# Optimization experiments

Measured on AMD Instinct MI355X. Metric: run time of the kernel, lower is better.

The kernel has to match this reference:

```python
import jax, jax.numpy as jnp
import numpy as np

NEG_SLOPE = 0.2
EPS = 1e-16


def gat_layer(x, src, dst, W, att_src, att_dst, bias, heads, out_ch, concat, n_nodes):
    # Linear projection -> [N, H, C]
    h = (x @ W).reshape(n_nodes, heads, out_ch)
    # Per-node attention logits [N, H]
    a_src = (h * att_src[None]).sum(-1)
    a_dst = (h * att_dst[None]).sum(-1)
    # Per-edge logits, LeakyReLU (message j -> i with src=j, dst=i)
    alpha = a_src[src] + a_dst[dst]                      # [E, H]
    alpha = jnp.where(alpha >= 0, alpha, NEG_SLOPE * alpha)
    # Segment softmax over incoming edges of each dst node
    amax = jax.ops.segment_max(alpha, dst, num_segments=n_nodes)  # [N, H]
    ealpha = jnp.exp(alpha - amax[dst])
    denom = jax.ops.segment_sum(ealpha, dst, num_segments=n_nodes)
    alpha = ealpha / (denom[dst] + EPS)
    # Weighted messages + scatter-add aggregation
    msg = h[src] * alpha[..., None]                      # [E, H, C]
    out = jax.ops.segment_sum(msg, dst, num_segments=n_nodes)  # [N, H, C]
    out = out.reshape(n_nodes, heads * out_ch) if concat else out.mean(axis=1)
    return out + bias


def setup_inputs() -> dict:
    key = jax.random.key(0)
    ks = jax.random.split(key, 11)
    N, E, F, H, C1 = 50000, 1600000, 128, 8, 8
    x = jax.random.normal(ks[0], (N, F), dtype=jnp.float32)
    edge_index = jax.random.randint(ks[1], (2, E), 0, N, dtype=jnp.int64)
    s = 1.0 / np.sqrt(F)
    W1 = jax.random.normal(ks[2], (F, H * C1), dtype=jnp.float32) * s
    att_src1 = jax.random.normal(ks[3], (H, C1), dtype=jnp.float32) * 0.1
    att_dst1 = jax.random.normal(ks[4], (H, C1), dtype=jnp.float32) * 0.1
    bias1 = jax.random.normal(ks[5], (H * C1,), dtype=jnp.float32) * 0.1
    W2 = jax.random.normal(ks[6], (H * C1, F), dtype=jnp.float32) * (1.0 / np.sqrt(H * C1))
    att_src2 = jax.random.normal(ks[7], (1, F), dtype=jnp.float32) * 0.1
    att_dst2 = jax.random.normal(ks[8], (1, F), dtype=jnp.float32) * 0.1
    bias2 = jax.random.normal(ks[9], (F,), dtype=jnp.float32) * 0.1
    return {"x": x, "edge_index": edge_index, "W1": W1, "att_src1": att_src1,
            "att_dst1": att_dst1, "bias1": bias1, "W2": W2, "att_src2": att_src2,
            "att_dst2": att_dst2, "bias2": bias2}


def reference(x, edge_index, W1, att_src1, att_dst1, bias1, W2, att_src2, att_dst2, bias2):
    N = x.shape[0]
    # PyG GATConv add_self_loops=True: append (i, i) for every node
    loops = jnp.arange(N, dtype=edge_index.dtype)
    src = jnp.concatenate([edge_index[0], loops])
    dst = jnp.concatenate([edge_index[1], loops])
    # eval mode: dropouts are identity
    h = gat_layer(x, src, dst, W1, att_src1, att_dst1, bias1, heads=8, out_ch=8,
                  concat=True, n_nodes=N)            # [N, 64]
    h = jax.nn.elu(h)
    out = gat_layer(h, src, dst, W2, att_src2, att_dst2, bias2, heads=1, out_ch=128,
                    concat=False, n_nodes=N)         # [N, 128]
    return out
```

## Files before the change

### kernel.cpp

```cpp
#include <hip/hip_runtime.h>
#include <stdint.h>

#define NEG_SLOPE 0.2f
#define EPSV 1e-16f
#define NBLK 256

typedef __attribute__((ext_vector_type(8))) short short8;
typedef __attribute__((ext_vector_type(4))) float f32x4;

__device__ inline short bf16r(float f){
  union { float f; unsigned u; } v; v.f = f;
  unsigned r = (v.u + 0x7FFFu + ((v.u >> 16) & 1u)) >> 16;
  return (short)r;
}
__device__ inline float bf16lo(unsigned u){
  union { unsigned u; float f; } v; v.u = u << 16; return v.f;
}
__device__ inline float bf16hi(unsigned u){
  union { unsigned u; float f; } v; v.u = u & 0xFFFF0000u; return v.f;
}

__device__ inline void get_edge(const void* ei, int is64, int E, int e, int& s, int& d){
  if (e >= E){ s = d = e - E; return; }
  if (is64){
    const long long* p = (const long long*)ei;
    s = (int)p[e]; d = (int)p[(long long)E + e];
  } else {
    const int* p = (const int*)ei;
    s = p[e]; d = p[E + e];
  }
}

__device__ inline int get_dst(const void* ei, int is64, int E, int e){
  if (e >= E) return e - E;
  if (is64) return (int)((const long long*)ei)[(long long)E + e];
  return ((const int*)ei)[E + e];
}

__global__ void detect_dtype(const int* ei32, int* flag){
  if (threadIdx.x == 0 && blockIdx.x == 0){
    int nz = 0;
    for (int i = 0; i < 64; ++i) nz |= ei32[2*i + 1];
    *flag = (nz == 0) ? 1 : 0;
  }
}

__global__ void cvt_to_bf16(const float* __restrict__ x, short* __restrict__ xb, int n4){
  int i = blockIdx.x*blockDim.x + threadIdx.x;
  if (i >= n4) return;
  f32x4 v = *(const f32x4*)(x + (size_t)i*4);
  short4 o;
  o.x = bf16r(v[0]); o.y = bf16r(v[1]); o.z = bf16r(v[2]); o.w = bf16r(v[3]);
  *(short4*)(xb + (size_t)i*4) = o;
}

__device__ inline void pack_one(const float* W, short* Wp, int NCOL, int idx){
  int NNT = NCOL >> 4;
  int j = idx & 7, n16 = (idx >> 3) & 15, q = (idx >> 7) & 3, tile = idx >> 9;
  int nt = tile % NNT, kt = tile / NNT;
  int k = kt*32 + q*8 + j, n = nt*16 + n16;
  Wp[idx] = bf16r(W[k*NCOL + n]);
}
__global__ void pack_w_both(const float* __restrict__ W1, short* __restrict__ W1p,
                            const float* __restrict__ W2, short* __restrict__ W2p){
  int idx = blockIdx.x*blockDim.x + threadIdx.x;
  if (idx < 8192) pack_one(W1, W1p, 64, idx);
  else            pack_one(W2, W2p, 128, idx - 8192);
}

__global__ void gemv_att2(const float* __restrict__ W2, const float* __restrict__ as2,
                          const float* __restrict__ ad2, float* __restrict__ va_s,
                          float* __restrict__ va_d){
  int k = threadIdx.x;
  float s = 0.f, d = 0.f;
  for (int c = 0; c < 128; ++c){
    float w = W2[k*128 + c];
    s = fmaf(w, as2[c], s);
    d = fmaf(w, ad2[c], d);
  }
  va_s[k] = s; va_d[k] = d;
}

template<int K, int NCOL>
__global__ __launch_bounds__(256) void gemm_mfma(const short* __restrict__ A, const short* __restrict__ Bp,
                                                 short* __restrict__ Cb, int M){
  constexpr int NKT = K/32, NNT = NCOL/16;
  int wave = (blockIdx.x*256 + (int)threadIdx.x) >> 6;
  int lane = threadIdx.x & 63;
  int row0 = wave << 4;
  if (row0 >= M) return;
  int m = lane & 15, q = lane >> 4;
  f32x4 acc[NNT];
#pragma unroll
  for (int i = 0; i < NNT; ++i) acc[i] = (f32x4){0.f,0.f,0.f,0.f};
#pragma unroll
  for (int kt = 0; kt < NKT; ++kt){
    short8 a = *(const short8*)(A + (size_t)(row0 + m)*K + kt*32 + q*8);
#pragma unroll
    for (int nt = 0; nt < NNT; ++nt){
      short8 b = *(const short8*)(Bp + (size_t)(((kt*NNT + nt)*4 + q)*16 + m)*8);
      acc[nt] = __builtin_amdgcn_mfma_f32_16x16x32_bf16(a, b, acc[nt], 0, 0, 0);
    }
  }
#pragma unroll
  for (int nt = 0; nt < NNT; ++nt){
#pragma unroll
    for (int r = 0; r < 4; ++r){
      Cb[(size_t)(row0 + q*4 + r)*NCOL + nt*16 + m] = bf16r(acc[nt][r]);
    }
  }
}

template<int K, int NCOL>
__global__ __launch_bounds__(256) void gemm_mfma_bias(const short* __restrict__ A, const short* __restrict__ Bp,
                                                      const float* __restrict__ bias,
                                                      float* __restrict__ C, int M){
  constexpr int NKT = K/32, NNT = NCOL/16;
  int wave = (blockIdx.x*256 + (int)threadIdx.x) >> 6;
  int lane = threadIdx.x & 63;
  int row0 = wave << 4;
  if (row0 >= M) return;
  int m = lane & 15, q = lane >> 4;
  f32x4 acc[NNT];
#pragma unroll
  for (int i = 0; i < NNT; ++i) acc[i] = (f32x4){0.f,0.f,0.f,0.f};
#pragma unroll
  for (int kt = 0; kt < NKT; ++kt){
    short8 a = *(const short8*)(A + (size_t)(row0 + m)*K + kt*32 + q*8);
#pragma unroll
    for (int nt = 0; nt < NNT; ++nt){
      short8 b = *(const short8*)(Bp + (size_t)(((kt*NNT + nt)*4 + q)*16 + m)*8);
      acc[nt] = __builtin_amdgcn_mfma_f32_16x16x32_bf16(a, b, acc[nt], 0, 0, 0);
    }
  }
#pragma unroll
  for (int nt = 0; nt < NNT; ++nt){
    float bv = bias[nt*16 + m];
#pragma unroll
    for (int r = 0; r < 4; ++r){
      C[(size_t)(row0 + q*4 + r)*NCOL + nt*16 + m] = acc[nt][r] + bv;
    }
  }
}

__global__ void logits_l1(const unsigned short* __restrict__ h1b, const float* __restrict__ att_s,
                          const float* __restrict__ att_d, float* __restrict__ asrc,
                          float* __restrict__ adst, int N){
  int tid = threadIdx.x;
  int n = blockIdx.x*4 + (tid >> 6);
  int j = tid & 63;
  if (n >= N) return;
  float h = bf16lo((unsigned)h1b[(size_t)n*64 + j]);
  float ps = h * att_s[j];
  float pd = h * att_d[j];
#pragma unroll
  for (int mm = 4; mm; mm >>= 1){ ps += __shfl_xor(ps, mm, 8); pd += __shfl_xor(pd, mm, 8); }
  if ((j & 7) == 0){ asrc[n*8 + (j >> 3)] = ps; adst[n*8 + (j >> 3)] = pd; }
}

__global__ __launch_bounds__(256) void p1_hist(const void* ei, const int* flag, int E, int E2,
                                               int* __restrict__ block_counts){
  __shared__ int h[256];
  int t = threadIdx.x, blk = blockIdx.x;
  h[t] = 0; __syncthreads();
  int chunk = (E2 + NBLK - 1)/NBLK;
  int beg = blk*chunk, end = min(beg + chunk, E2);
  int is64 = *flag;
  for (int e = beg + t; e < end; e += 256){
    int d = get_dst(ei, is64, E, e);
    atomicAdd(&h[d >> 8], 1);
  }
  __syncthreads();
  block_counts[blk*256 + t] = h[t];
}

__global__ void p2_bucket_scan(const int* __restrict__ block_counts, int* __restrict__ bucket_base){
  __shared__ int sd[256];
  int t = threadIdx.x;
  int tot = 0;
  for (int b = 0; b < NBLK; ++b) tot += block_counts[b*256 + t];
  sd[t] = tot; __syncthreads();
  for (int off = 1; off < 256; off <<= 1){
    int v = (t >= off) ? sd[t - off] : 0;
    __syncthreads(); sd[t] += v; __syncthreads();
  }
  bucket_base[t] = sd[t] - tot;
  if (t == 255) bucket_base[256] = sd[255];
}

__global__ void p2_block_off(const int* __restrict__ block_counts, const int* __restrict__ bucket_base,
                             int* __restrict__ block_off){
  __shared__ int sd[256];
  int b = blockIdx.x, t = threadIdx.x;
  int v = block_counts[t*256 + b];
  sd[t] = v; __syncthreads();
  for (int off = 1; off < 256; off <<= 1){
    int u = (t >= off) ? sd[t - off] : 0;
    __syncthreads(); sd[t] += u; __syncthreads();
  }
  block_off[t*256 + b] = bucket_base[b] + sd[t] - v;
}

__global__ __launch_bounds__(256) void p3_scatter(const void* ei, const int* flag, int E, int E2,
                                                  const int* __restrict__ block_off,
                                                  unsigned* __restrict__ packed){
  __shared__ int cur[256];
  int t = threadIdx.x, blk = blockIdx.x;
  cur[t] = block_off[blk*256 + t];
  __syncthreads();
  int chunk = (E2 + NBLK - 1)/NBLK;
  int beg = blk*chunk, end = min(beg + chunk, E2);
  int is64 = *flag;
  for (int e = beg + t; e < end; e += 256){
    int s, d; get_edge(ei, is64, E, e, s, d);
    int pos = atomicAdd(&cur[d >> 8], 1);
    packed[pos] = ((unsigned)s << 8) | (unsigned)(d & 255);
  }
}

__global__ __launch_bounds__(256) void p4_sort(const unsigned* __restrict__ packed,
                                               const int* __restrict__ bucket_base,
                                               int N, int E2,
                                               int* __restrict__ offs, int* __restrict__ srcs){
  __shared__ int hist[256];
  __shared__ int cur[256];
  int b = blockIdx.x, t = threadIdx.x;
  int base = bucket_base[b], cnt = bucket_base[b + 1] - base;
  hist[t] = 0; __syncthreads();
  for (int p = t; p < cnt; p += 256){
    atomicAdd(&hist[packed[base + p] & 255u], 1);
  }
  __syncthreads();
  int v = hist[t];
  cur[t] = v; __syncthreads();
  for (int off = 1; off < 256; off <<= 1){
    int u = (t >= off) ? cur[t - off] : 0;
    __syncthreads(); cur[t] += u; __syncthreads();
  }
  int ex = cur[t] - v;
  __syncthreads();
  cur[t] = ex;
  int node = b*256 + t;
  if (node < N) offs[node] = base + ex;
  __syncthreads();
  for (int p = t; p < cnt; p += 256){
    unsigned pk = packed[base + p];
    int pos = atomicAdd(&cur[pk & 255u], 1);
    srcs[base + pos] = (int)(pk >> 8);
  }
  if (b == 0 && t == 0) offs[N] = E2;
}

__global__ __launch_bounds__(256) void agg_l1(const char* __restrict__ h1b,
                       const float* __restrict__ asrc, const float* __restrict__ adst,
                       const int* __restrict__ offs, const int* __restrict__ srcs,
                       const float* __restrict__ bias,
                       const float* __restrict__ va_s, const float* __restrict__ va_d,
                       uint4* __restrict__ hout,
                       float* __restrict__ asrc2, float* __restrict__ adst2, int N){
  int tid = threadIdx.x;
  int i = blockIdx.x*4 + (tid >> 6);
  if (i >= N) return;
  int lane = tid & 63, g = lane >> 3, c = lane & 7;
  float ad = adst[i*8 + c];
  int beg = offs[i], end = offs[i + 1], last = end - 1;
  float acc[8];
#pragma unroll
  for (int k = 0; k < 8; ++k) acc[k] = 0.f;
  float den = 0.f;
  for (int p = beg; p < end; p += 32){
    int m[4], s[4];
#pragma unroll
    for (int k = 0; k < 4; ++k) m[k] = p + 8*k + g;
#pragma unroll
    for (int k = 0; k < 4; ++k) s[k] = srcs[min(m[k], last)];
    float a[4];
#pragma unroll
    for (int k = 0; k < 4; ++k) a[k] = asrc[s[k]*8 + c];
    uint4 v[4];
#pragma unroll
    for (int k = 0; k < 4; ++k) v[k] = *(const uint4*)(h1b + ((size_t)s[k] << 7) + (c << 4));
    float w[4];
#pragma unroll
    for (int k = 0; k < 4; ++k){
      float z = a[k] + ad; z = (z >= 0.f) ? z : NEG_SLOPE*z;
      w[k] = (m[k] < end) ? __expf(z) : 0.f;
      den += w[k];
    }
#pragma unroll
    for (int k = 0; k < 4; ++k){
      acc[0] = fmaf(w[k], bf16lo(v[k].x), acc[0]); acc[1] = fmaf(w[k], bf16hi(v[k].x), acc[1]);
      acc[2] = fmaf(w[k], bf16lo(v[k].y), acc[2]); acc[3] = fmaf(w[k], bf16hi(v[k].y), acc[3]);
      acc[4] = fmaf(w[k], bf16lo(v[k].z), acc[4]); acc[5] = fmaf(w[k], bf16hi(v[k].z), acc[5]);
      acc[6] = fmaf(w[k], bf16lo(v[k].w), acc[6]); acc[7] = fmaf(w[k], bf16hi(v[k].w), acc[7]);
    }
  }
#pragma unroll
  for (int mm = 8; mm <= 32; mm <<= 1){
#pragma unroll
    for (int k = 0; k < 8; ++k) acc[k] += __shfl_xor(acc[k], mm, 64);
    den += __shfl_xor(den, mm, 64);
  }
  if (g == 0){
    float inv = 1.f/(den + EPSV);
    float o[8];
#pragma unroll
    for (int k = 0; k < 8; ++k){
      float t = acc[k]*inv + bias[c*8 + k];
      o[k] = (t > 0.f) ? t : (__expf(t) - 1.f);
    }
    unsigned pk[4];
#pragma unroll
    for (int k = 0; k < 4; ++k)
      pk[k] = (unsigned)(unsigned short)bf16r(o[2*k]) | ((unsigned)(unsigned short)bf16r(o[2*k+1]) << 16);
    uint4 ov; ov.x = pk[0]; ov.y = pk[1]; ov.z = pk[2]; ov.w = pk[3];
    hout[(size_t)i*8 + c] = ov;
    float ps = 0.f, pd = 0.f;
#pragma unroll
    for (int k = 0; k < 8; ++k){
      ps = fmaf(o[k], va_s[c*8 + k], ps);
      pd = fmaf(o[k], va_d[c*8 + k], pd);
    }
#pragma unroll
    for (int mm = 1; mm <= 4; mm <<= 1){
      ps += __shfl_xor(ps, mm, 8);
      pd += __shfl_xor(pd, mm, 8);
    }
    if (c == 0){ asrc2[i] = ps; adst2[i] = pd; }
  }
}

__global__ __launch_bounds__(256) void agg_l2(const char* __restrict__ hin2,
                       const float* __restrict__ asrc, const float* __restrict__ adst,
                       const int* __restrict__ offs, const int* __restrict__ srcs,
                       uint4* __restrict__ qout, int N){
  int tid = threadIdx.x;
  int i = blockIdx.x*4 + (tid >> 6);
  if (i >= N) return;
  int lane = tid & 63, g = lane >> 3, c = lane & 7;
  float ad = adst[i];
  int beg = offs[i], end = offs[i + 1], last = end - 1;
  float acc[8];
#pragma unroll
  for (int k = 0; k < 8; ++k) acc[k] = 0.f;
  float den = 0.f;
  for (int p = beg; p < end; p += 32){
    int m[4], s[4];
#pragma unroll
    for (int k = 0; k < 4; ++k) m[k] = p + 8*k + g;
#pragma unroll
    for (int k = 0; k < 4; ++k) s[k] = srcs[min(m[k], last)];
    float a[4];
#pragma unroll
    for (int k = 0; k < 4; ++k) a[k] = asrc[s[k]];
    uint4 v[4];
#pragma unroll
    for (int k = 0; k < 4; ++k) v[k] = *(const uint4*)(hin2 + ((size_t)s[k] << 7) + (c << 4));
    float w[4];
#pragma unroll
    for (int k = 0; k < 4; ++k){
      float z = a[k] + ad; z = (z >= 0.f) ? z : NEG_SLOPE*z;
      w[k] = (m[k] < end) ? __expf(z) : 0.f;
      den += w[k];
    }
#pragma unroll
    for (int k = 0; k < 4; ++k){
      acc[0] = fmaf(w[k], bf16lo(v[k].x), acc[0]); acc[1] = fmaf(w[k], bf16hi(v[k].x), acc[1]);
      acc[2] = fmaf(w[k], bf16lo(v[k].y), acc[2]); acc[3] = fmaf(w[k], bf16hi(v[k].y), acc[3]);
      acc[4] = fmaf(w[k], bf16lo(v[k].z), acc[4]); acc[5] = fmaf(w[k], bf16hi(v[k].z), acc[5]);
      acc[6] = fmaf(w[k], bf16lo(v[k].w), acc[6]); acc[7] = fmaf(w[k], bf16hi(v[k].w), acc[7]);
    }
  }
#pragma unroll
  for (int mm = 8; mm <= 32; mm <<= 1){
#pragma unroll
    for (int k = 0; k < 8; ++k) acc[k] += __shfl_xor(acc[k], mm, 64);
    den += __shfl_xor(den, mm, 64);
  }
  if (g == 0){
    float inv = 1.f/(den + EPSV);
    unsigned pk[4];
#pragma unroll
    for (int k = 0; k < 4; ++k){
      float o0 = acc[2*k]*inv, o1 = acc[2*k + 1]*inv;
      pk[k] = (unsigned)(unsigned short)bf16r(o0) | ((unsigned)(unsigned short)bf16r(o1) << 16);
    }
    uint4 ov; ov.x = pk[0]; ov.y = pk[1]; ov.z = pk[2]; ov.w = pk[3];
    qout[(size_t)i*8 + c] = ov;
  }
}

extern "C" void kernel_launch(void* const* d_in, const int* in_sizes, int n_in,
                              void* d_out, int out_size, void* d_ws, size_t ws_size,
                              hipStream_t stream){
  const float* x   = (const float*)d_in[0];
  const void*  ei  = d_in[1];
  const float* W1  = (const float*)d_in[2];
  const float* as1 = (const float*)d_in[3];
  const float* ad1 = (const float*)d_in[4];
  const float* b1  = (const float*)d_in[5];
  const float* W2  = (const float*)d_in[6];
  const float* as2 = (const float*)d_in[7];
  const float* ad2 = (const float*)d_in[8];
  const float* b2  = (const float*)d_in[9];

  int N  = in_sizes[0] / 128;
  int E  = in_sizes[1] / 2;
  int E2 = E + N;
  int NB = (N + 255) >> 8;

  char* p = (char*)d_ws;
  auto alloc = [&](size_t bytes) -> void* {
    void* r = (void*)p;
    p += (bytes + 255) & ~(size_t)255;
    return r;
  };
  short*    xb     = (short*)alloc((size_t)N*128*2);
  short*    W1p    = (short*)alloc((size_t)128*64*2);
  short*    W2p    = (short*)alloc((size_t)64*128*2);
  short*    h1b    = (short*)alloc((size_t)N*64*2);
  float*    asrc1  = (float*)alloc((size_t)N*8*4);
  float*    adst1  = (float*)alloc((size_t)N*8*4);
  short*    hin2   = (short*)alloc((size_t)N*64*2);
  short*    hq     = (short*)alloc((size_t)N*64*2);
  float*    asrc2  = (float*)alloc((size_t)N*4);
  float*    adst2  = (float*)alloc((size_t)N*4);
  float*    va_s2  = (float*)alloc(64*4);
  float*    va_d2  = (float*)alloc(64*4);
  int*      offs   = (int*)alloc((size_t)(N + 1)*4);
  int*      srcs   = (int*)alloc((size_t)E2*4);
  unsigned* packed = (unsigned*)alloc((size_t)E2*4);
  int*      bcnt   = (int*)alloc((size_t)NBLK*256*4);
  int*      boff   = (int*)alloc((size_t)NBLK*256*4);
  int*      bbase  = (int*)alloc(257*4);
  int*      flag   = (int*)alloc(4);

  dim3 B(256);
  detect_dtype<<<1, 64, 0, stream>>>((const int*)ei, flag);

  int n4 = N*128/4;
  cvt_to_bf16<<<(n4 + 255)/256, B, 0, stream>>>(x, xb, n4);
  pack_w_both<<<16384/256, B, 0, stream>>>(W1, W1p, W2, W2p);
  gemv_att2<<<1, 64, 0, stream>>>(W2, as2, ad2, va_s2, va_d2);

  int nwav = (N + 15)/16;
  gemm_mfma<128,64><<<(nwav + 3)/4, B, 0, stream>>>(xb, W1p, h1b, N);
  logits_l1<<<(N + 3)/4, B, 0, stream>>>((const unsigned short*)h1b, as1, ad1, asrc1, adst1, N);

  p1_hist<<<NBLK, B, 0, stream>>>(ei, flag, E, E2, bcnt);
  p2_bucket_scan<<<1, B, 0, stream>>>(bcnt, bbase);
  p2_block_off<<<256, B, 0, stream>>>(bcnt, bbase, boff);
  p3_scatter<<<NBLK, B, 0, stream>>>(ei, flag, E, E2, boff, packed);
  p4_sort<<<NB, B, 0, stream>>>(packed, bbase, N, E2, offs, srcs);

  agg_l1<<<(N + 3)/4, B, 0, stream>>>((const char*)h1b, asrc1, adst1, offs, srcs, b1,
                                      va_s2, va_d2, (uint4*)hin2, asrc2, adst2, N);

  agg_l2<<<(N + 3)/4, B, 0, stream>>>((const char*)hin2, asrc2, adst2, offs, srcs,
                                      (uint4*)hq, N);

  gemm_mfma_bias<64,128><<<(nwav + 3)/4, B, 0, stream>>>(hq, W2p, b2, (float*)d_out, N);
}
```

Before: 254.2 us.

## Fuse prep kernels, bf16 convert into GEMM1, logits into GEMM epilogue, merge scans

Merges the dtype check, weight packing and attention GEMV into one prep kernel. Folds the fp32-to-bf16 conversion of x into the first GEMM's A load and computes the layer-1 attention logits in that GEMM's epilogue using shuffles. Merges the two scan kernels into one, which makes every block redo the bucket totals. Pre-scales logits by log2(e) so aggregation can use exp2f, and stores pre-shifted source offsets to save index arithmetic. The aim is fewer launches and less intermediate memory traffic, at the cost of redundant per-block scan work.

```diff
diff --git a/kernel.cpp b/kernel.cpp
--- a/kernel.cpp
+++ b/kernel.cpp
@@ -3,6 +3,7 @@
 
 #define NEG_SLOPE 0.2f
 #define EPSV 1e-16f
+#define LOG2E 1.44269504088896340736f
 #define NBLK 256
 
 typedef __attribute__((ext_vector_type(8))) short short8;
@@ -37,23 +38,6 @@
   return ((const int*)ei)[E + e];
 }
 
-__global__ void detect_dtype(const int* ei32, int* flag){
-  if (threadIdx.x == 0 && blockIdx.x == 0){
-    int nz = 0;
-    for (int i = 0; i < 64; ++i) nz |= ei32[2*i + 1];
-    *flag = (nz == 0) ? 1 : 0;
-  }
-}
-
-__global__ void cvt_to_bf16(const float* __restrict__ x, short* __restrict__ xb, int n4){
-  int i = blockIdx.x*blockDim.x + threadIdx.x;
-  if (i >= n4) return;
-  f32x4 v = *(const f32x4*)(x + (size_t)i*4);
-  short4 o;
-  o.x = bf16r(v[0]); o.y = bf16r(v[1]); o.z = bf16r(v[2]); o.w = bf16r(v[3]);
-  *(short4*)(xb + (size_t)i*4) = o;
-}
-
 __device__ inline void pack_one(const float* W, short* Wp, int NCOL, int idx){
   int NNT = NCOL >> 4;
   int j = idx & 7, n16 = (idx >> 3) & 15, q = (idx >> 7) & 3, tile = idx >> 9;
@@ -61,30 +45,39 @@
   int k = kt*32 + q*8 + j, n = nt*16 + n16;
   Wp[idx] = bf16r(W[k*NCOL + n]);
 }
-__global__ void pack_w_both(const float* __restrict__ W1, short* __restrict__ W1p,
-                            const float* __restrict__ W2, short* __restrict__ W2p){
-  int idx = blockIdx.x*blockDim.x + threadIdx.x;
-  if (idx < 8192) pack_one(W1, W1p, 64, idx);
-  else            pack_one(W2, W2p, 128, idx - 8192);
-}
-
-__global__ void gemv_att2(const float* __restrict__ W2, const float* __restrict__ as2,
-                          const float* __restrict__ ad2, float* __restrict__ va_s,
-                          float* __restrict__ va_d){
-  int k = threadIdx.x;
-  float s = 0.f, d = 0.f;
-  for (int c = 0; c < 128; ++c){
-    float w = W2[k*128 + c];
-    s = fmaf(w, as2[c], s);
-    d = fmaf(w, ad2[c], d);
-  }
-  va_s[k] = s; va_d[k] = d;
-}
-
-template<int K, int NCOL>
-__global__ __launch_bounds__(256) void gemm_mfma(const short* __restrict__ A, const short* __restrict__ Bp,
-                                                 short* __restrict__ Cb, int M){
-  constexpr int NKT = K/32, NNT = NCOL/16;
+__global__ void prep(const int* __restrict__ ei32, int* __restrict__ flag,
+                     const float* __restrict__ W1, short* __restrict__ W1p,
+                     const float* __restrict__ W2, short* __restrict__ W2p,
+                     const float* __restrict__ as2, const float* __restrict__ ad2,
+                     float* __restrict__ va_s, float* __restrict__ va_d){
+  int b = blockIdx.x, t = threadIdx.x;
+  if (b < 64){
+    int idx = b*256 + t;
+    if (idx < 8192) pack_one(W1, W1p, 64, idx);
+    else            pack_one(W2, W2p, 128, idx - 8192);
+  } else {
+    if (t == 0){
+      int nz = 0;
+      for (int i = 0; i < 64; ++i) nz |= ei32[2*i + 1];
+      *flag = (nz == 0) ? 1 : 0;
+    }
+    if (t < 64){
+      float s = 0.f, d = 0.f;
+      for (int c = 0; c < 128; ++c){
+        float w = W2[t*128 + c];
+        s = fmaf(w, as2[c], s);
+        d = fmaf(w, ad2[c], d);
+      }
+      va_s[t] = s * LOG2E; va_d[t] = d * LOG2E;
+    }
+  }
+}
+
+__global__ __launch_bounds__(256) void gemm1(const float* __restrict__ x, const short* __restrict__ Bp,
+                                             const float* __restrict__ att_s, const float* __restrict__ att_d,
+                                             short* __restrict__ Cb,
+                                             float* __restrict__ asrc1, float* __restrict__ adst1, int M){
+  constexpr int NKT = 4, NNT = 4;
   int wave = (blockIdx.x*256 + (int)threadIdx.x) >> 6;
   int lane = threadIdx.x & 63;
   int row0 = wave << 4;
@@ -95,7 +88,12 @@
   for (int i = 0; i < NNT; ++i) acc[i] = (f32x4){0.f,0.f,0.f,0.f};
 #pragma unroll
   for (int kt = 0; kt < NKT; ++kt){
-    short8 a = *(const short8*)(A + (size_t)(row0 + m)*K + kt*32 + q*8);
+    const float* xr = x + (size_t)(row0 + m)*128 + kt*32 + q*8;
+    f32x4 f0 = *(const f32x4*)xr;
+    f32x4 f1 = *(const f32x4*)(xr + 4);
+    short8 a;
+#pragma unroll
+    for (int j = 0; j < 4; ++j){ a[j] = bf16r(f0[j]); a[4 + j] = bf16r(f1[j]); }
 #pragma unroll
     for (int nt = 0; nt < NNT; ++nt){
       short8 b = *(const short8*)(Bp + (size_t)(((kt*NNT + nt)*4 + q)*16 + m)*8);
@@ -106,16 +104,41 @@
   for (int nt = 0; nt < NNT; ++nt){
 #pragma unroll
     for (int r = 0; r < 4; ++r){
-      Cb[(size_t)(row0 + q*4 + r)*NCOL + nt*16 + m] = bf16r(acc[nt][r]);
-    }
-  }
-}
-
-template<int K, int NCOL>
-__global__ __launch_bounds__(256) void gemm_mfma_bias(const short* __restrict__ A, const short* __restrict__ Bp,
-                                                      const float* __restrict__ bias,
-                                                      float* __restrict__ C, int M){
-  constexpr int NKT = K/32, NNT = NCOL/16;
+      Cb[(size_t)(row0 + q*4 + r)*64 + nt*16 + m] = bf16r(acc[nt][r]);
+    }
+  }
+  float atts[4], attd[4];
+#pragma unroll
+  for (int nt = 0; nt < 4; ++nt){
+    atts[nt] = att_s[nt*16 + m] * LOG2E;
+    attd[nt] = att_d[nt*16 + m] * LOG2E;
+  }
+  int isw = (m & 7) == 0;
+#pragma unroll
+  for (int r = 0; r < 4; ++r){
+    int row = row0 + q*4 + r;
+#pragma unroll
+    for (int nt = 0; nt < 4; ++nt){
+      float ps = acc[nt][r] * atts[nt];
+      float pd = acc[nt][r] * attd[nt];
+#pragma unroll
+      for (int mm = 1; mm <= 4; mm <<= 1){
+        ps += __shfl_xor(ps, mm, 64);
+        pd += __shfl_xor(pd, mm, 64);
+      }
+      if (isw){
+        int head = 2*nt + (m >> 3);
+        asrc1[row*8 + head] = ps;
+        adst1[row*8 + head] = pd;
+      }
+    }
+  }
+}
+
+__global__ __launch_bounds__(256) void gemm2(const short* __restrict__ A, const short* __restrict__ Bp,
+                                             const float* __restrict__ bias,
+                                             float* __restrict__ C, int M){
+  constexpr int NKT = 2, NNT = 8;
   int wave = (blockIdx.x*256 + (int)threadIdx.x) >> 6;
   int lane = threadIdx.x & 63;
   int row0 = wave << 4;
@@ -126,7 +149,7 @@
   for (int i = 0; i < NNT; ++i) acc[i] = (f32x4){0.f,0.f,0.f,0.f};
 #pragma unroll
   for (int kt = 0; kt < NKT; ++kt){
-    short8 a = *(const short8*)(A + (size_t)(row0 + m)*K + kt*32 + q*8);
+    short8 a = *(const short8*)(A + (size_t)(row0 + m)*64 + kt*32 + q*8);
 #pragma unroll
     for (int nt = 0; nt < NNT; ++nt){
       short8 b = *(const short8*)(Bp + (size_t)(((kt*NNT + nt)*4 + q)*16 + m)*8);
@@ -138,24 +161,9 @@
     float bv = bias[nt*16 + m];
 #pragma unroll
     for (int r = 0; r < 4; ++r){
-      C[(size_t)(row0 + q*4 + r)*NCOL + nt*16 + m] = acc[nt][r] + bv;
-    }
-  }
-}
-
-__global__ void logits_l1(const unsigned short* __restrict__ h1b, const float* __restrict__ att_s,
-                          const float* __restrict__ att_d, float* __restrict__ asrc,
-                          float* __restrict__ adst, int N){
-  int tid = threadIdx.x;
-  int n = blockIdx.x*4 + (tid >> 6);
-  int j = tid & 63;
-  if (n >= N) return;
-  float h = bf16lo((unsigned)h1b[(size_t)n*64 + j]);
-  float ps = h * att_s[j];
-  float pd = h * att_d[j];
-#pragma unroll
-  for (int mm = 4; mm; mm >>= 1){ ps += __shfl_xor(ps, mm, 8); pd += __shfl_xor(pd, mm, 8); }
-  if ((j & 7) == 0){ asrc[n*8 + (j >> 3)] = ps; adst[n*8 + (j >> 3)] = pd; }
+      C[(size_t)(row0 + q*4 + r)*128 + nt*16 + m] = acc[nt][r] + bv;
+    }
+  }
 }
 
 __global__ __launch_bounds__(256) void p1_hist(const void* ei, const int* flag, int E, int E2,
@@ -174,31 +182,34 @@
   block_counts[blk*256 + t] = h[t];
 }
 
-__global__ void p2_bucket_scan(const int* __restrict__ block_counts, int* __restrict__ bucket_base){
-  __shared__ int sd[256];
-  int t = threadIdx.x;
-  int tot = 0;
-  for (int b = 0; b < NBLK; ++b) tot += block_counts[b*256 + t];
-  sd[t] = tot; __syncthreads();
+__global__ __launch_bounds__(256) void p2_scan(const int* __restrict__ block_counts,
+                                               int* __restrict__ bucket_base,
+                                               int* __restrict__ block_off){
+  __shared__ int tot[256];
+  __shared__ int ex[256];
+  __shared__ int col[256];
+  int b = blockIdx.x, t = threadIdx.x;
+  int s = 0;
+  for (int w = 0; w < NBLK; ++w) s += block_counts[w*256 + t];
+  tot[t] = s; __syncthreads();
   for (int off = 1; off < 256; off <<= 1){
-    int v = (t >= off) ? sd[t - off] : 0;
-    __syncthreads(); sd[t] += v; __syncthreads();
-  }
-  bucket_base[t] = sd[t] - tot;
-  if (t == 255) bucket_base[256] = sd[255];
-}
-
-__global__ void p2_block_off(const int* __restrict__ block_counts, const int* __restrict__ bucket_base,
-                             int* __restrict__ block_off){
-  __shared__ int sd[256];
-  int b = blockIdx.x, t = threadIdx.x;
+    int v = (t >= off) ? tot[t - off] : 0;
+    __syncthreads(); tot[t] += v; __syncthreads();
+  }
+  ex[t] = tot[t] - s;
+  __syncthreads();
+  if (b == 0){
+    bucket_base[t] = ex[t];
+    if (t == 255) bucket_base[256] = tot[255];
+  }
+  int base = ex[b];
   int v = block_counts[t*256 + b];
-  sd[t] = v; __syncthreads();
+  col[t] = v; __syncthreads();
   for (int off = 1; off < 256; off <<= 1){
-    int u = (t >= off) ? sd[t - off] : 0;
-    __syncthreads(); sd[t] += u; __syncthreads();
-  }
-  block_off[t*256 + b] = bucket_base[b] + sd[t] - v;
+    int u = (t >= off) ? col[t - off] : 0;
+    __syncthreads(); col[t] += u; __syncthreads();
+  }
+  block_off[t*256 + b] = base + col[t] - v;
 }
 
 __global__ __launch_bounds__(256) void p3_scatter(const void* ei, const int* flag, int E, int E2,
@@ -246,7 +257,7 @@
   for (int p = t; p < cnt; p += 256){
     unsigned pk = packed[base + p];
     int pos = atomicAdd(&cur[pk & 255u], 1);
-    srcs[base + pos] = (int)(pk >> 8);
+    srcs[base + pos] = (int)((pk >> 8) << 7);
   }
   if (b == 0 && t == 0) offs[N] = E2;
 }
@@ -262,6 +273,7 @@
   int i = blockIdx.x*4 + (tid >> 6);
   if (i >= N) return;
   int lane = tid & 63, g = lane >> 3, c = lane & 7;
+  unsigned coff = (unsigned)(c << 4);
   float ad = adst[i*8 + c];
   int beg = offs[i], end = offs[i + 1], last = end - 1;
   float acc[8];
@@ -269,22 +281,23 @@
   for (int k = 0; k < 8; ++k) acc[k] = 0.f;
   float den = 0.f;
   for (int p = beg; p < end; p += 32){
-    int m[4], s[4];
+    int m[4]; unsigned so[4];
 #pragma unroll
     for (int k = 0; k < 4; ++k) m[k] = p + 8*k + g;
 #pragma unroll
-    for (int k = 0; k < 4; ++k) s[k] = srcs[min(m[k], last)];
+    for (int k = 0; k < 4; ++k) so[k] = (unsigned)srcs[min(m[k], last)];
     float a[4];
 #pragma unroll
-    for (int k = 0; k < 4; ++k) a[k] = asrc[s[k]*8 + c];
+    for (int k = 0; k < 4; ++k) a[k] = asrc[(so[k] >> 4) + (unsigned)c];
     uint4 v[4];
 #pragma unroll
-    for (int k = 0; k < 4; ++k) v[k] = *(const uint4*)(h1b + ((size_t)s[k] << 7) + (c << 4));
+    for (int k = 0; k < 4; ++k) v[k] = *(const uint4*)(h1b + (size_t)(so[k] + coff));
     float w[4];
 #pragma unroll
     for (int k = 0; k < 4; ++k){
-      float z = a[k] + ad; z = (z >= 0.f) ? z : NEG_SLOPE*z;
-      w[k] = (m[k] < end) ? __expf(z) : 0.f;
+      float z = a[k] + ad;
+      z = fmaxf(z, NEG_SLOPE*z);
+      w[k] = (m[k] < end) ? exp2f(z) : 0.f;
       den += w[k];
     }
 #pragma unroll
@@ -338,6 +351,7 @@
   int i = blockIdx.x*4 + (tid >> 6);
   if (i >= N) return;
   int lane = tid & 63, g = lane >> 3, c = lane & 7;
+  unsigned coff = (unsigned)(c << 4);
   float ad = adst[i];
   int beg = offs[i], end = offs[i + 1], last = end - 1;
   float acc[8];
@@ -345,22 +359,23 @@
   for (int k = 0; k < 8; ++k) acc[k] = 0.f;
   float den = 0.f;
   for (int p = beg; p < end; p += 32){
-    int m[4], s[4];
+    int m[4]; unsigned so[4];
 #pragma unroll
     for (int k = 0; k < 4; ++k) m[k] = p + 8*k + g;
 #pragma unroll
-    for (int k = 0; k < 4; ++k) s[k] = srcs[min(m[k], last)];
+    for (int k = 0; k < 4; ++k) so[k] = (unsigned)srcs[min(m[k], last)];
     float a[4];
 #pragma unroll
-    for (int k = 0; k < 4; ++k) a[k] = asrc[s[k]];
+    for (int k = 0; k < 4; ++k) a[k] = asrc[so[k] >> 7];
     uint4 v[4];
 #pragma unroll
-    for (int k = 0; k < 4; ++k) v[k] = *(const uint4*)(hin2 + ((size_t)s[k] << 7) + (c << 4));
+    for (int k = 0; k < 4; ++k) v[k] = *(const uint4*)(hin2 + (size_t)(so[k] + coff));
     float w[4];
 #pragma unroll
     for (int k = 0; k < 4; ++k){
-      float z = a[k] + ad; z = (z >= 0.f) ? z : NEG_SLOPE*z;
-      w[k] = (m[k] < end) ? __expf(z) : 0.f;
+      float z = a[k] + ad;
+      z = fmaxf(z, NEG_SLOPE*z);
+      w[k] = (m[k] < end) ? exp2f(z) : 0.f;
       den += w[k];
     }
 #pragma unroll
@@ -415,7 +430,6 @@
     p += (bytes + 255) & ~(size_t)255;
     return r;
   };
-  short*    xb     = (short*)alloc((size_t)N*128*2);
   short*    W1p    = (short*)alloc((size_t)128*64*2);
   short*    W2p    = (short*)alloc((size_t)64*128*2);
   short*    h1b    = (short*)alloc((size_t)N*64*2);
@@ -436,20 +450,13 @@
   int*      flag   = (int*)alloc(4);
 
   dim3 B(256);
-  detect_dtype<<<1, 64, 0, stream>>>((const int*)ei, flag);
-
-  int n4 = N*128/4;
-  cvt_to_bf16<<<(n4 + 255)/256, B, 0, stream>>>(x, xb, n4);
-  pack_w_both<<<16384/256, B, 0, stream>>>(W1, W1p, W2, W2p);
-  gemv_att2<<<1, 64, 0, stream>>>(W2, as2, ad2, va_s2, va_d2);
+  prep<<<65, B, 0, stream>>>((const int*)ei, flag, W1, W1p, W2, W2p, as2, ad2, va_s2, va_d2);
 
   int nwav = (N + 15)/16;
-  gemm_mfma<128,64><<<(nwav + 3)/4, B, 0, stream>>>(xb, W1p, h1b, N);
-  logits_l1<<<(N + 3)/4, B, 0, stream>>>((const unsigned short*)h1b, as1, ad1, asrc1, adst1, N);
+  gemm1<<<(nwav + 3)/4, B, 0, stream>>>(x, W1p, as1, ad1, h1b, asrc1, adst1, N);
 
   p1_hist<<<NBLK, B, 0, stream>>>(ei, flag, E, E2, bcnt);
-  p2_bucket_scan<<<1, B, 0, stream>>>(bcnt, bbase);
-  p2_block_off<<<256, B, 0, stream>>>(bcnt, bbase, boff);
+  p2_scan<<<256, B, 0, stream>>>(bcnt, bbase, boff);
   p3_scatter<<<NBLK, B, 0, stream>>>(ei, flag, E, E2, boff, packed);
   p4_sort<<<NB, B, 0, stream>>>(packed, bbase, N, E2, offs, srcs);
 
@@ -459,5 +466,5 @@
   agg_l2<<<(N + 3)/4, B, 0, stream>>>((const char*)hin2, asrc2, adst2, offs, srcs,
                                       (uint4*)hq, N);
 
-  gemm_mfma_bias<64,128><<<(nwav + 3)/4, B, 0, stream>>>(hq, W2p, b2, (float*)d_out, N);
-}
+  gemm2<<<(nwav + 3)/4, B, 0, stream>>>(hq, W2p, b2, (float*)d_out, N);
+}
```

After: 243.0 us. 1.05x faster.
